# Performance work log

Hardware: AMD Instinct MI355X
Metric: run time of the kernel (lower is better)

Reference implementation:

```python
import jax, jax.numpy as jnp
import numpy as np

D = 2048       # hidden_size
F = 8192       # intermediate_size
R = 16         # flylora_rank
SCALING = 32.0 / R   # alpha / rank = 2.0
GAMMA = 0.1


def _era(x):
    # ERA(x) = GELU_tanh(x) + gamma * softplus(x)
    return jax.nn.gelu(x, approximate=True) + GAMMA * jax.nn.softplus(x)


def setup_inputs() -> dict:
    key = jax.random.key(0)
    ks = jax.random.split(key, 16)
    s = 0.02
    inp = {
        'x': jax.random.normal(ks[0], (4, 2048, D), dtype=jnp.float32),
        # gate FlyLoRA (weights stored [in, out])
        'Wg':  jax.random.normal(ks[1], (D, F), dtype=jnp.float32) * s,
        'bg':  jnp.zeros((F,), jnp.float32),
        'Wgd': jax.random.normal(ks[2], (D, R), dtype=jnp.float32) * s,
        'bgd': jnp.zeros((R,), jnp.float32),
        'Wgu': jax.random.normal(ks[3], (R, F), dtype=jnp.float32) * s,
        'bgu': jnp.zeros((F,), jnp.float32),
        # up FlyLoRA
        'Wu':  jax.random.normal(ks[4], (D, F), dtype=jnp.float32) * s,
        'bu':  jnp.zeros((F,), jnp.float32),
        'Wud': jax.random.normal(ks[5], (D, R), dtype=jnp.float32) * s,
        'bud': jnp.zeros((R,), jnp.float32),
        'Wuu': jax.random.normal(ks[6], (R, F), dtype=jnp.float32) * s,
        'buu': jnp.zeros((F,), jnp.float32),
        # down_proj
        'Wd':  jax.random.normal(ks[7], (F, D), dtype=jnp.float32) * s,
        'bd':  jnp.zeros((D,), jnp.float32),
    }
    return inp


def _flylora(x, W, b, Wdn, bdn, Wup, bup):
    # base(x) + scaling * lora_up(lora_down(x))
    base = jnp.einsum('bsd,df->bsf', x, W) + b
    lora = jnp.einsum('bsr,rf->bsf', jnp.einsum('bsd,dr->bsr', x, Wdn) + bdn, Wup) + bup
    return base + SCALING * lora


def reference(x, Wg, bg, Wgd, bgd, Wgu, bgu, Wu, bu, Wud, bud, Wuu, buu, Wd, bd):
    gate = _era(_flylora(x, Wg, bg, Wgd, bgd, Wgu, bgu))
    up = _flylora(x, Wu, bu, Wud, bud, Wuu, buu)
    return jnp.einsum('bsf,fd->bsd', gate * up, Wd) + bd
```

## Files before the change

### kernel.cpp

```cpp
#include <hip/hip_runtime.h>
#include <cstdint>
#include <cstddef>

#define D_DIM 2048
#define F_DIM 8192
#define M_DIM 8192
#define SCALING 2.0f
#define GAMMA 0.1f
#define LDS_PITCH 40

typedef __bf16 bf16x8 __attribute__((ext_vector_type(8)));
typedef float f32x4 __attribute__((ext_vector_type(4)));
typedef unsigned short ushort_t;

__device__ __forceinline__ unsigned short f2bf(float f) {
  unsigned int u = __float_as_uint(f);
  u += 0x7FFF + ((u >> 16) & 1);
  return (unsigned short)(u >> 16);
}

__device__ __forceinline__ float era_f(float x) {
  float x3 = x * x * x;
  float inner = 0.7978845608028654f * (x + 0.044715f * x3);
  float e = __expf(2.0f * inner);
  float th = 1.0f - 2.0f / (e + 1.0f);
  float gelu = 0.5f * x * (1.0f + th);
  float sp = fmaxf(x, 0.0f) + __logf(1.0f + __expf(-fabsf(x)));
  return gelu + GAMMA * sp;
}


__global__ void convert_x(const float* __restrict__ in, ushort_t* __restrict__ out, int n) {
  int i = (blockIdx.x * 256 + threadIdx.x) * 4;
  if (i >= n) return;
  float4 v = *(const float4*)(in + i);
  out[i + 0] = f2bf(v.x);
  out[i + 1] = f2bf(v.y);
  out[i + 2] = f2bf(v.z);
  out[i + 3] = f2bf(v.w);
}

__global__ void transpose_w(const float* __restrict__ in, ushort_t* __restrict__ out,
                            int K, int N) {
  __shared__ float tile[32][33];
  int k0 = blockIdx.y * 32, n0 = blockIdx.x * 32;
  int tr = threadIdx.x >> 5, tc = threadIdx.x & 31;
#pragma unroll
  for (int i = 0; i < 32; i += 8)
    tile[tr + i][tc] = in[(size_t)(k0 + tr + i) * N + n0 + tc];
  __syncthreads();
#pragma unroll
  for (int i = 0; i < 32; i += 8)
    out[(size_t)(n0 + tr + i) * K + k0 + tc] = f2bf(tile[tc][tr + i]);
}

__global__ void pad_small(const float* __restrict__ in, ushort_t* __restrict__ out, int F) {
  int idx = blockIdx.x * 256 + threadIdx.x;
  int f = idx >> 5, k = idx & 31;
  float v = (k < 16) ? in[(size_t)k * F + f] : 0.0f;
  out[idx] = f2bf(v);
}

__global__ void lora_down(const float* __restrict__ x,
                          const float* __restrict__ Wgd, const float* __restrict__ bgd,
                          const float* __restrict__ Wud, const float* __restrict__ bud,
                          ushort_t* __restrict__ xdg, ushort_t* __restrict__ xdu) {
  int row = blockIdx.x * 8 + (threadIdx.x >> 5);
  int c = threadIdx.x & 31;
  bool isG = (c < 16);
  int col = c & 15;
  const float* W = isG ? Wgd : Wud;
  const float* xr = x + (size_t)row * D_DIM;
  float acc = 0.0f;
  for (int k = 0; k < D_DIM; ++k)
    acc = fmaf(xr[k], W[k * 16 + col], acc);
  float b = isG ? bgd[col] : bud[col];
  ushort_t v = f2bf(SCALING * (acc + b));
  ushort_t* dst = isG ? xdg : xdu;
  dst[row * 32 + col] = v;
  dst[row * 32 + 16 + col] = 0;
}


__device__ __forceinline__ void stage_tile(ushort_t* dst, const ushort_t* src, int ldK) {
  int t = threadIdx.x;
#pragma unroll
  for (int p = 0; p < 2; ++p) {
    int idx = t + p * 256;
    int row = idx >> 2;
    int ch = idx & 3;
    uint4 v = *(const uint4*)(src + (size_t)row * ldK + ch * 8);
    *(uint4*)(dst + row * LDS_PITCH + ch * 8) = v;
  }
}

__device__ __forceinline__ bf16x8 frag_ld(const ushort_t* lds, int row, int q) {
  union { uint4 u; bf16x8 v; } un;
  un.u = *(const uint4*)(lds + row * LDS_PITCH + q * 8);
  return un.v;
}

__global__ __launch_bounds__(256) void gemm_gateup(
    const ushort_t* __restrict__ xbf, const ushort_t* __restrict__ Wgt,
    const ushort_t* __restrict__ Wut, const ushort_t* __restrict__ Wgup,
    const ushort_t* __restrict__ Wuup, const ushort_t* __restrict__ xdg,
    const ushort_t* __restrict__ xdu,
    const float* __restrict__ bg, const float* __restrict__ bgu,
    const float* __restrict__ bu, const float* __restrict__ buu,
    ushort_t* __restrict__ tout) {
  __shared__ ushort_t xs[128 * LDS_PITCH];
  __shared__ ushort_t wgs[128 * LDS_PITCH];
  __shared__ ushort_t wus[128 * LDS_PITCH];
  const int f0 = blockIdx.x * 128;
  const int m0 = blockIdx.y * 128;
  const int w = threadIdx.x >> 6, lane = threadIdx.x & 63;
  const int wm = w >> 1, wn = w & 1;
  const int ml = lane & 15, q = lane >> 4;

  const f32x4 zero4 = {0.f, 0.f, 0.f, 0.f};
  f32x4 accg[4][4], accu[4][4];
#pragma unroll
  for (int i = 0; i < 4; ++i)
#pragma unroll
    for (int j = 0; j < 4; ++j) { accg[i][j] = zero4; accu[i][j] = zero4; }

  const ushort_t* xsrc = xbf + (size_t)m0 * D_DIM;
  const ushort_t* gsrc = Wgt + (size_t)f0 * D_DIM;
  const ushort_t* usrc = Wut + (size_t)f0 * D_DIM;

  for (int kt = 0; kt < D_DIM / 32; ++kt) {
    __syncthreads();
    stage_tile(xs, xsrc + kt * 32, D_DIM);
    stage_tile(wgs, gsrc + kt * 32, D_DIM);
    stage_tile(wus, usrc + kt * 32, D_DIM);
    __syncthreads();
    bf16x8 af[4], bgf[4], buf2[4];
#pragma unroll
    for (int i = 0; i < 4; ++i) {
      af[i]   = frag_ld(xs,  wm * 64 + i * 16 + ml, q);
      bgf[i]  = frag_ld(wgs, wn * 64 + i * 16 + ml, q);
      buf2[i] = frag_ld(wus, wn * 64 + i * 16 + ml, q);
    }
#pragma unroll
    for (int mi = 0; mi < 4; ++mi)
#pragma unroll
      for (int ni = 0; ni < 4; ++ni) {
        accg[mi][ni] = __builtin_amdgcn_mfma_f32_16x16x32_bf16(af[mi], bgf[ni], accg[mi][ni], 0, 0, 0);
        accu[mi][ni] = __builtin_amdgcn_mfma_f32_16x16x32_bf16(af[mi], buf2[ni], accu[mi][ni], 0, 0, 0);
      }
  }

  __syncthreads();
  stage_tile(xs, xdg + (size_t)m0 * 32, 32);
  stage_tile(wgs, Wgup + (size_t)f0 * 32, 32);
  __syncthreads();
  {
    bf16x8 af[4], bgf[4];
#pragma unroll
    for (int i = 0; i < 4; ++i) {
      af[i]  = frag_ld(xs,  wm * 64 + i * 16 + ml, q);
      bgf[i] = frag_ld(wgs, wn * 64 + i * 16 + ml, q);
    }
#pragma unroll
    for (int mi = 0; mi < 4; ++mi)
#pragma unroll
      for (int ni = 0; ni < 4; ++ni)
        accg[mi][ni] = __builtin_amdgcn_mfma_f32_16x16x32_bf16(af[mi], bgf[ni], accg[mi][ni], 0, 0, 0);
  }
  __syncthreads();
  stage_tile(xs, xdu + (size_t)m0 * 32, 32);
  stage_tile(wus, Wuup + (size_t)f0 * 32, 32);
  __syncthreads();
  {
    bf16x8 af[4], buf2[4];
#pragma unroll
    for (int i = 0; i < 4; ++i) {
      af[i]   = frag_ld(xs,  wm * 64 + i * 16 + ml, q);
      buf2[i] = frag_ld(wus, wn * 64 + i * 16 + ml, q);
    }
#pragma unroll
    for (int mi = 0; mi < 4; ++mi)
#pragma unroll
      for (int ni = 0; ni < 4; ++ni)
        accu[mi][ni] = __builtin_amdgcn_mfma_f32_16x16x32_bf16(af[mi], buf2[ni], accu[mi][ni], 0, 0, 0);
  }

#pragma unroll
  for (int ni = 0; ni < 4; ++ni) {
    int col = f0 + wn * 64 + ni * 16 + ml;
    float cbg = bg[col] + SCALING * bgu[col];
    float cbu = bu[col] + SCALING * buu[col];
#pragma unroll
    for (int mi = 0; mi < 4; ++mi) {
      int row0 = m0 + wm * 64 + mi * 16 + q * 4;
#pragma unroll
      for (int r = 0; r < 4; ++r) {
        float hg = accg[mi][ni][r] + cbg;
        float hu = accu[mi][ni][r] + cbu;
        tout[(size_t)(row0 + r) * F_DIM + col] = f2bf(era_f(hg) * hu);
      }
    }
  }
}

__global__ __launch_bounds__(256) void gemm_down(
    const ushort_t* __restrict__ tin, const ushort_t* __restrict__ Wdt,
    const float* __restrict__ bd, float* __restrict__ out) {
  __shared__ ushort_t as_[128 * LDS_PITCH];
  __shared__ ushort_t bs_[128 * LDS_PITCH];
  const int n0 = blockIdx.x * 128;
  const int m0 = blockIdx.y * 128;
  const int w = threadIdx.x >> 6, lane = threadIdx.x & 63;
  const int wm = w >> 1, wn = w & 1;
  const int ml = lane & 15, q = lane >> 4;

  const f32x4 zero4 = {0.f, 0.f, 0.f, 0.f};
  f32x4 acc[4][4];
#pragma unroll
  for (int i = 0; i < 4; ++i)
#pragma unroll
    for (int j = 0; j < 4; ++j) acc[i][j] = zero4;

  const ushort_t* asrc = tin + (size_t)m0 * F_DIM;
  const ushort_t* bsrc = Wdt + (size_t)n0 * F_DIM;

  for (int kt = 0; kt < F_DIM / 32; ++kt) {
    __syncthreads();
    stage_tile(as_, asrc + kt * 32, F_DIM);
    stage_tile(bs_, bsrc + kt * 32, F_DIM);
    __syncthreads();
    bf16x8 af[4], bf_[4];
#pragma unroll
    for (int i = 0; i < 4; ++i) {
      af[i]  = frag_ld(as_, wm * 64 + i * 16 + ml, q);
      bf_[i] = frag_ld(bs_, wn * 64 + i * 16 + ml, q);
    }
#pragma unroll
    for (int mi = 0; mi < 4; ++mi)
#pragma unroll
      for (int ni = 0; ni < 4; ++ni)
        acc[mi][ni] = __builtin_amdgcn_mfma_f32_16x16x32_bf16(af[mi], bf_[ni], acc[mi][ni], 0, 0, 0);
  }

#pragma unroll
  for (int ni = 0; ni < 4; ++ni) {
    int col = n0 + wn * 64 + ni * 16 + ml;
    float b = bd[col];
#pragma unroll
    for (int mi = 0; mi < 4; ++mi) {
      int row0 = m0 + wm * 64 + mi * 16 + q * 4;
#pragma unroll
      for (int r = 0; r < 4; ++r)
        out[(size_t)(row0 + r) * D_DIM + col] = acc[mi][ni][r] + b;
    }
  }
}


extern "C" void kernel_launch(void* const* d_in, const int* in_sizes, int n_in,
                              void* d_out, int out_size, void* d_ws, size_t ws_size,
                              hipStream_t stream) {
  const float* x   = (const float*)d_in[0];
  const float* Wg  = (const float*)d_in[1];
  const float* bg  = (const float*)d_in[2];
  const float* Wgd = (const float*)d_in[3];
  const float* bgd = (const float*)d_in[4];
  const float* Wgu = (const float*)d_in[5];
  const float* bgu = (const float*)d_in[6];
  const float* Wu  = (const float*)d_in[7];
  const float* bu  = (const float*)d_in[8];
  const float* Wud = (const float*)d_in[9];
  const float* bud = (const float*)d_in[10];
  const float* Wuu = (const float*)d_in[11];
  const float* buu = (const float*)d_in[12];
  const float* Wd  = (const float*)d_in[13];
  const float* bd  = (const float*)d_in[14];
  float* out = (float*)d_out;

  char* ws = (char*)d_ws;
  size_t off = 0;
  auto alloc = [&](size_t bytes) {
    char* p = ws + off;
    off += (bytes + 255) & ~(size_t)255;
    return p;
  };
  ushort_t* xbf  = (ushort_t*)alloc((size_t)M_DIM * D_DIM * 2);
  ushort_t* Wgt  = (ushort_t*)alloc((size_t)F_DIM * D_DIM * 2);
  ushort_t* Wut  = (ushort_t*)alloc((size_t)F_DIM * D_DIM * 2);
  ushort_t* Wdt  = (ushort_t*)alloc((size_t)D_DIM * F_DIM * 2);
  ushort_t* Wgup = (ushort_t*)alloc((size_t)F_DIM * 32 * 2);
  ushort_t* Wuup = (ushort_t*)alloc((size_t)F_DIM * 32 * 2);
  ushort_t* xdg  = (ushort_t*)alloc((size_t)M_DIM * 32 * 2);
  ushort_t* xdu  = (ushort_t*)alloc((size_t)M_DIM * 32 * 2);
  ushort_t* tbuf = (ushort_t*)alloc((size_t)M_DIM * F_DIM * 2);

  convert_x<<<(M_DIM * D_DIM / 4 + 255) / 256, 256, 0, stream>>>(x, xbf, M_DIM * D_DIM);
  transpose_w<<<dim3(F_DIM / 32, D_DIM / 32), 256, 0, stream>>>(Wg, Wgt, D_DIM, F_DIM);
  transpose_w<<<dim3(F_DIM / 32, D_DIM / 32), 256, 0, stream>>>(Wu, Wut, D_DIM, F_DIM);
  transpose_w<<<dim3(D_DIM / 32, F_DIM / 32), 256, 0, stream>>>(Wd, Wdt, F_DIM, D_DIM);
  pad_small<<<F_DIM * 32 / 256, 256, 0, stream>>>(Wgu, Wgup, F_DIM);
  pad_small<<<F_DIM * 32 / 256, 256, 0, stream>>>(Wuu, Wuup, F_DIM);
  lora_down<<<M_DIM / 8, 256, 0, stream>>>(x, Wgd, bgd, Wud, bud, xdg, xdu);
  gemm_gateup<<<dim3(F_DIM / 128, M_DIM / 128), 256, 0, stream>>>(
      xbf, Wgt, Wut, Wgup, Wuup, xdg, xdu, bg, bgu, bu, buu, tbuf);
  gemm_down<<<dim3(D_DIM / 128, M_DIM / 128), 256, 0, stream>>>(tbuf, Wdt, bd, out);
}
```

Measured before the change: 1.617 ms.

## Stage GEMM tiles via direct global-to-LDS loads with XOR-swizzled layout

Both GEMM kernels now copy tiles straight from global memory into LDS with 16-byte global_load_lds, replacing loads that went through registers and then back out to LDS. Because these direct loads write each wave's lanes contiguously, the padded LDS pitch is replaced by a dense 32-element row with an XOR swizzle. The swizzle is applied on the global source column and undone on the fragment read to limit bank conflicts. This should cut VGPR use and per-tile instruction count. The loop is still single-buffered with two barriers per k-step, so load latency is still not overlapped with compute.

```diff
diff --git a/kernel.cpp b/kernel.cpp
--- a/kernel.cpp
+++ b/kernel.cpp
@@ -7,7 +7,6 @@
 #define M_DIM 8192
 #define SCALING 2.0f
 #define GAMMA 0.1f
-#define LDS_PITCH 40
 
 typedef __bf16 bf16x8 __attribute__((ext_vector_type(8)));
 typedef float f32x4 __attribute__((ext_vector_type(4)));
@@ -82,23 +81,18 @@
 }
 
 
-__device__ __forceinline__ void stage_tile(ushort_t* dst, const ushort_t* src, int ldK) {
-  int t = threadIdx.x;
-#pragma unroll
-  for (int p = 0; p < 2; ++p) {
-    int idx = t + p * 256;
-    int row = idx >> 2;
-    int ch = idx & 3;
-    uint4 v = *(const uint4*)(src + (size_t)row * ldK + ch * 8);
-    *(uint4*)(dst + row * LDS_PITCH + ch * 8) = v;
-  }
-}
-
-__device__ __forceinline__ bf16x8 frag_ld(const ushort_t* lds, int row, int q) {
+__device__ __forceinline__ void gload16(const ushort_t* g, ushort_t* l) {
+  __builtin_amdgcn_global_load_lds(
+      (__attribute__((address_space(1))) void*)g,
+      (__attribute__((address_space(3))) void*)l, 16, 0, 0);
+}
+
+__device__ __forceinline__ bf16x8 frag_ld(const ushort_t* p) {
   union { uint4 u; bf16x8 v; } un;
-  un.u = *(const uint4*)(lds + row * LDS_PITCH + q * 8);
+  un.u = *(const uint4*)p;
   return un.v;
 }
+
 
 __global__ __launch_bounds__(256) void gemm_gateup(
     const ushort_t* __restrict__ xbf, const ushort_t* __restrict__ Wgt,
@@ -108,15 +102,24 @@
     const float* __restrict__ bg, const float* __restrict__ bgu,
     const float* __restrict__ bu, const float* __restrict__ buu,
     ushort_t* __restrict__ tout) {
-  __shared__ ushort_t xs[128 * LDS_PITCH];
-  __shared__ ushort_t wgs[128 * LDS_PITCH];
-  __shared__ ushort_t wus[128 * LDS_PITCH];
+  __shared__ __align__(16) ushort_t xs[128 * 32];
+  __shared__ __align__(16) ushort_t wgs[128 * 32];
+  __shared__ __align__(16) ushort_t wus[128 * 32];
   const int f0 = blockIdx.x * 128;
   const int m0 = blockIdx.y * 128;
-  const int w = threadIdx.x >> 6, lane = threadIdx.x & 63;
+  const int t = threadIdx.x;
+  const int w = t >> 6, lane = t & 63;
   const int wm = w >> 1, wn = w & 1;
   const int ml = lane & 15, q = lane >> 4;
 
+  const int srow = t >> 2;
+  const int cs = ((t & 3) ^ ((srow >> 1) & 3)) * 8;
+  const int slotq = (q ^ ((ml >> 1) & 3)) * 8;
+
+  ushort_t* xd0 = xs + w * 512;   ushort_t* xd1 = xs + 2048 + w * 512;
+  ushort_t* gd0 = wgs + w * 512;  ushort_t* gd1 = wgs + 2048 + w * 512;
+  ushort_t* ud0 = wus + w * 512;  ushort_t* ud1 = wus + 2048 + w * 512;
+
   const f32x4 zero4 = {0.f, 0.f, 0.f, 0.f};
   f32x4 accg[4][4], accu[4][4];
 #pragma unroll
@@ -124,22 +127,26 @@
 #pragma unroll
     for (int j = 0; j < 4; ++j) { accg[i][j] = zero4; accu[i][j] = zero4; }
 
-  const ushort_t* xsrc = xbf + (size_t)m0 * D_DIM;
-  const ushort_t* gsrc = Wgt + (size_t)f0 * D_DIM;
-  const ushort_t* usrc = Wut + (size_t)f0 * D_DIM;
+  const ushort_t* xsrc0 = xbf + (size_t)(m0 + srow) * D_DIM + cs;
+  const ushort_t* xsrc1 = xsrc0 + (size_t)64 * D_DIM;
+  const ushort_t* gsrc0 = Wgt + (size_t)(f0 + srow) * D_DIM + cs;
+  const ushort_t* gsrc1 = gsrc0 + (size_t)64 * D_DIM;
+  const ushort_t* usrc0 = Wut + (size_t)(f0 + srow) * D_DIM + cs;
+  const ushort_t* usrc1 = usrc0 + (size_t)64 * D_DIM;
 
   for (int kt = 0; kt < D_DIM / 32; ++kt) {
+    const int ko = kt * 32;
     __syncthreads();
-    stage_tile(xs, xsrc + kt * 32, D_DIM);
-    stage_tile(wgs, gsrc + kt * 32, D_DIM);
-    stage_tile(wus, usrc + kt * 32, D_DIM);
+    gload16(xsrc0 + ko, xd0);  gload16(xsrc1 + ko, xd1);
+    gload16(gsrc0 + ko, gd0);  gload16(gsrc1 + ko, gd1);
+    gload16(usrc0 + ko, ud0);  gload16(usrc1 + ko, ud1);
     __syncthreads();
     bf16x8 af[4], bgf[4], buf2[4];
 #pragma unroll
     for (int i = 0; i < 4; ++i) {
-      af[i]   = frag_ld(xs,  wm * 64 + i * 16 + ml, q);
-      bgf[i]  = frag_ld(wgs, wn * 64 + i * 16 + ml, q);
-      buf2[i] = frag_ld(wus, wn * 64 + i * 16 + ml, q);
+      af[i]   = frag_ld(xs  + (wm * 64 + i * 16 + ml) * 32 + slotq);
+      bgf[i]  = frag_ld(wgs + (wn * 64 + i * 16 + ml) * 32 + slotq);
+      buf2[i] = frag_ld(wus + (wn * 64 + i * 16 + ml) * 32 + slotq);
     }
 #pragma unroll
     for (int mi = 0; mi < 4; ++mi)
@@ -151,15 +158,17 @@
   }
 
   __syncthreads();
-  stage_tile(xs, xdg + (size_t)m0 * 32, 32);
-  stage_tile(wgs, Wgup + (size_t)f0 * 32, 32);
+  gload16(xdg + ((size_t)m0 + srow) * 32 + cs, xd0);
+  gload16(xdg + ((size_t)m0 + srow + 64) * 32 + cs, xd1);
+  gload16(Wgup + ((size_t)f0 + srow) * 32 + cs, gd0);
+  gload16(Wgup + ((size_t)f0 + srow + 64) * 32 + cs, gd1);
   __syncthreads();
   {
     bf16x8 af[4], bgf[4];
 #pragma unroll
     for (int i = 0; i < 4; ++i) {
-      af[i]  = frag_ld(xs,  wm * 64 + i * 16 + ml, q);
-      bgf[i] = frag_ld(wgs, wn * 64 + i * 16 + ml, q);
+      af[i]  = frag_ld(xs  + (wm * 64 + i * 16 + ml) * 32 + slotq);
+      bgf[i] = frag_ld(wgs + (wn * 64 + i * 16 + ml) * 32 + slotq);
     }
 #pragma unroll
     for (int mi = 0; mi < 4; ++mi)
@@ -168,15 +177,17 @@
         accg[mi][ni] = __builtin_amdgcn_mfma_f32_16x16x32_bf16(af[mi], bgf[ni], accg[mi][ni], 0, 0, 0);
   }
   __syncthreads();
-  stage_tile(xs, xdu + (size_t)m0 * 32, 32);
-  stage_tile(wus, Wuup + (size_t)f0 * 32, 32);
+  gload16(xdu + ((size_t)m0 + srow) * 32 + cs, xd0);
+  gload16(xdu + ((size_t)m0 + srow + 64) * 32 + cs, xd1);
+  gload16(Wuup + ((size_t)f0 + srow) * 32 + cs, ud0);
+  gload16(Wuup + ((size_t)f0 + srow + 64) * 32 + cs, ud1);
   __syncthreads();
   {
     bf16x8 af[4], buf2[4];
 #pragma unroll
     for (int i = 0; i < 4; ++i) {
-      af[i]   = frag_ld(xs,  wm * 64 + i * 16 + ml, q);
-      buf2[i] = frag_ld(wus, wn * 64 + i * 16 + ml, q);
+      af[i]   = frag_ld(xs  + (wm * 64 + i * 16 + ml) * 32 + slotq);
+      buf2[i] = frag_ld(wus + (wn * 64 + i * 16 + ml) * 32 + slotq);
     }
 #pragma unroll
     for (int mi = 0; mi < 4; ++mi)
@@ -206,14 +217,22 @@
 __global__ __launch_bounds__(256) void gemm_down(
     const ushort_t* __restrict__ tin, const ushort_t* __restrict__ Wdt,
     const float* __restrict__ bd, float* __restrict__ out) {
-  __shared__ ushort_t as_[128 * LDS_PITCH];
-  __shared__ ushort_t bs_[128 * LDS_PITCH];
+  __shared__ __align__(16) ushort_t as_[128 * 32];
+  __shared__ __align__(16) ushort_t bs_[128 * 32];
   const int n0 = blockIdx.x * 128;
   const int m0 = blockIdx.y * 128;
-  const int w = threadIdx.x >> 6, lane = threadIdx.x & 63;
+  const int t = threadIdx.x;
+  const int w = t >> 6, lane = t & 63;
   const int wm = w >> 1, wn = w & 1;
   const int ml = lane & 15, q = lane >> 4;
 
+  const int srow = t >> 2;
+  const int cs = ((t & 3) ^ ((srow >> 1) & 3)) * 8;
+  const int slotq = (q ^ ((ml >> 1) & 3)) * 8;
+
+  ushort_t* ad0 = as_ + w * 512;  ushort_t* ad1 = as_ + 2048 + w * 512;
+  ushort_t* bd0 = bs_ + w * 512;  ushort_t* bd1 = bs_ + 2048 + w * 512;
+
   const f32x4 zero4 = {0.f, 0.f, 0.f, 0.f};
   f32x4 acc[4][4];
 #pragma unroll
@@ -221,19 +240,22 @@
 #pragma unroll
     for (int j = 0; j < 4; ++j) acc[i][j] = zero4;
 
-  const ushort_t* asrc = tin + (size_t)m0 * F_DIM;
-  const ushort_t* bsrc = Wdt + (size_t)n0 * F_DIM;
+  const ushort_t* asrc0 = tin + (size_t)(m0 + srow) * F_DIM + cs;
+  const ushort_t* asrc1 = asrc0 + (size_t)64 * F_DIM;
+  const ushort_t* bsrc0 = Wdt + (size_t)(n0 + srow) * F_DIM + cs;
+  const ushort_t* bsrc1 = bsrc0 + (size_t)64 * F_DIM;
 
   for (int kt = 0; kt < F_DIM / 32; ++kt) {
+    const int ko = kt * 32;
     __syncthreads();
-    stage_tile(as_, asrc + kt * 32, F_DIM);
-    stage_tile(bs_, bsrc + kt * 32, F_DIM);
+    gload16(asrc0 + ko, ad0);  gload16(asrc1 + ko, ad1);
+    gload16(bsrc0 + ko, bd0);  gload16(bsrc1 + ko, bd1);
     __syncthreads();
     bf16x8 af[4], bf_[4];
 #pragma unroll
     for (int i = 0; i < 4; ++i) {
-      af[i]  = frag_ld(as_, wm * 64 + i * 16 + ml, q);
-      bf_[i] = frag_ld(bs_, wn * 64 + i * 16 + ml, q);
+      af[i]  = frag_ld(as_ + (wm * 64 + i * 16 + ml) * 32 + slotq);
+      bf_[i] = frag_ld(bs_ + (wn * 64 + i * 16 + ml) * 32 + slotq);
     }
 #pragma unroll
     for (int mi = 0; mi < 4; ++mi)
```

Measured after the change: 2.016 ms. +24.7%, slower.
